# Optimization experiments

Measured on AMD Instinct MI355X. Metric: run time of the kernel, lower is better.

Reference implementation:

```python
import jax, jax.numpy as jnp
import numpy as np

B, H, W, C = 16, 64, 64, 384
DH = 32                 # dim_head
NH = C // DH            # heads = dim // dim_head
WS = 8                  # window_size
DFF = 4 * C             # dim_ff default = 4*dim
EPS = 1e-5


def setup_inputs() -> dict:
    key = jax.random.key(0)
    ks = jax.random.split(key, 6)
    rn = lambda k, shape, scale: (jax.random.normal(k, shape, jnp.float32) * scale)
    return {
        "x": rn(ks[0], (B, H, W, C), 1.0),
        "w_qkv": rn(ks[1], (C, 3 * NH * DH), 0.02),   # fused qkv projection, bias=False
        "w_out": rn(ks[2], (NH * DH, C), 0.02),       # attention output projection
        "gamma_attn": jnp.ones((C,), jnp.float32),     # LayerNormNoBias2d weight (post-attn)
        "w1": rn(ks[3], (C, DFF), 0.02),               # FFN up projection
        "w2": rn(ks[4], (DFF, C), 0.02),               # FFN down projection
        "gamma_ff": jnp.ones((C,), jnp.float32),       # LayerNormNoBias2d weight (post-FFN)
    }


def _shift2d(x):
    # S2-MLP style 4-way spatial shift of channel quarters, zero-filled at borders.
    c4 = x.shape[-1] // 4
    g1 = jnp.pad(x[:, :-1, :, 0 * c4:1 * c4], ((0, 0), (1, 0), (0, 0), (0, 0)))  # shift down
    g2 = jnp.pad(x[:, 1:, :, 1 * c4:2 * c4], ((0, 0), (0, 1), (0, 0), (0, 0)))   # shift up
    g3 = jnp.pad(x[:, :, :-1, 2 * c4:3 * c4], ((0, 0), (0, 0), (1, 0), (0, 0)))  # shift right
    g4 = jnp.pad(x[:, :, 1:, 3 * c4:4 * c4], ((0, 0), (0, 0), (0, 1), (0, 0)))   # shift left
    return jnp.concatenate([g1, g2, g3, g4], axis=-1)


def _ln_nobias(x, gamma):
    # LayerNorm over channel dim, weight only (no bias).
    mu = jnp.mean(x, axis=-1, keepdims=True)
    var = jnp.var(x, axis=-1, keepdims=True)
    return (x - mu) * jax.lax.rsqrt(var + EPS) * gamma


def _window_attention(x, w_qkv, w_out):
    # Grouped (non-overlapping) window multi-head self-attention.
    b, h, w, c = x.shape
    nh, nw = h // WS, w // WS
    T = WS * WS
    # partition into windows: (b*nh*nw, T, c)
    xw = x.reshape(b, nh, WS, nw, WS, c).transpose(0, 1, 3, 2, 4, 5).reshape(b * nh * nw, T, c)
    qkv = xw @ w_qkv                                   # (n, T, 3*NH*DH)
    qkv = qkv.reshape(-1, T, 3, NH, DH)
    q = qkv[:, :, 0].transpose(0, 2, 1, 3)             # (n, NH, T, DH)
    k = qkv[:, :, 1].transpose(0, 2, 1, 3)
    v = qkv[:, :, 2].transpose(0, 2, 1, 3)
    logits = jnp.einsum('nhqd,nhkd->nhqk', q, k) * (DH ** -0.5)
    attn = jax.nn.softmax(logits, axis=-1)
    o = jnp.einsum('nhqk,nhkd->nhqd', attn, v)         # (n, NH, T, DH)
    o = o.transpose(0, 2, 1, 3).reshape(-1, T, NH * DH) @ w_out
    # un-window back to (b, h, w, c)
    return o.reshape(b, nh, nw, WS, WS, c).transpose(0, 1, 3, 2, 4, 5).reshape(b, h, w, c)


def reference(x, w_qkv, w_out, gamma_attn, w1, w2, gamma_ff):
    # x = x + DropBlock(Norm(GWAttn(Shift2d(x))))   (drop rates = 0 -> identity)
    a = _window_attention(_shift2d(x), w_qkv, w_out)
    x = x + _ln_nobias(a, gamma_attn)
    # x = x + DropBlock(Norm(FF(x)))
    f = jax.nn.gelu(x @ w1, approximate=False) @ w2
    return x + _ln_nobias(f, gamma_ff)
```

## Files before the change

kernel.cpp:

```cpp
#include <hip/hip_runtime.h>
#include <hip/hip_bf16.h>
#include <math.h>

typedef __attribute__((ext_vector_type(8))) __bf16 bf16x8;
typedef __attribute__((ext_vector_type(4))) float f32x4;
typedef unsigned int uint32;

static constexpr int kC   = 384;
static constexpr int kNH  = 12;
static constexpr int kDH  = 32;
static constexpr int kT   = 64;
static constexpr int kB   = 16;
static constexpr int kH   = 64;
static constexpr int kW   = 64;
static constexpr int kDFF = 1536;
static constexpr long kNTOK = 65536;
static constexpr long kNT  = kNTOK * kC;

__device__ __forceinline__ float bf_lo(uint32 u){ return __uint_as_float(u << 16); }
__device__ __forceinline__ float bf_hi(uint32 u){ return __uint_as_float(u & 0xffff0000u); }

__device__ __forceinline__ float gelu_fast(float x) {
    float x2 = x * x;
    float t  = fmaf(0.102944787f, x2, 2.302208165f);
    float m  = fminf(x * t, 80.0f);
    float e  = __builtin_amdgcn_exp2f(m);
    float d  = 1.0f + e;
    return x * e * __builtin_amdgcn_rcpf(d);
}

__global__ void k_transpose_cast(const float* __restrict__ src, __bf16* __restrict__ dst,
                                 int K, int N)
{
    int o = blockIdx.x * 256 + threadIdx.x;
    if (o >= K * N) return;
    int n = o / K, k = o - n * K;
    dst[o] = (__bf16)src[(size_t)k * N + n];
}

__global__ __launch_bounds__(256) void k_shift_window(const float* __restrict__ x,
                                                      __bf16* __restrict__ Aw)
{
    int tid = blockIdx.x * 256 + threadIdx.x;
    int m = tid / 48;
    int g = tid - m * 48;
    int c0 = g * 8;
    int wi = m >> 6, t = m & 63;
    int b = wi >> 6, nh = (wi >> 3) & 7, nw = wi & 7;
    int h = nh * 8 + (t >> 3);
    int w = nw * 8 + (t & 7);
    int q = c0 / 96;
    int sh = h, sw = w;
    bool ok;
    if      (q == 0) { sh = h - 1; ok = (h >= 1);  }
    else if (q == 1) { sh = h + 1; ok = (h <= 62); }
    else if (q == 2) { sw = w - 1; ok = (w >= 1);  }
    else             { sw = w + 1; ok = (w <= 62); }

    __bf16 r[8] __attribute__((aligned(16)));
    if (ok) {
        const float4* src = reinterpret_cast<const float4*>(
            x + (((size_t)b * kH + sh) * kW + sw) * kC + c0);
        float4 v0 = src[0], v1 = src[1];
        r[0] = (__bf16)v0.x; r[1] = (__bf16)v0.y; r[2] = (__bf16)v0.z; r[3] = (__bf16)v0.w;
        r[4] = (__bf16)v1.x; r[5] = (__bf16)v1.y; r[6] = (__bf16)v1.z; r[7] = (__bf16)v1.w;
    } else {
        #pragma unroll
        for (int i = 0; i < 8; ++i) r[i] = (__bf16)0.0f;
    }
    *reinterpret_cast<int4*>(Aw + (size_t)m * kC + c0) = *reinterpret_cast<int4*>(r);
}

template<int EPI>
__global__ __launch_bounds__(256) void k_gemm(const __bf16* __restrict__ A,
                                              const __bf16* __restrict__ B,
                                              __bf16* __restrict__ Cout,
                                              int N, int K, int nt)
{
    __shared__ __align__(16) __bf16 As[2][128 * 32];
    __shared__ __align__(16) __bf16 Bs[2][128 * 32];
    const int tid  = threadIdx.x;
    const int wave = tid >> 6, lane = tid & 63;
    const int g = lane >> 4, qh = lane & 15;

    const int nwg = gridDim.x;
    const int wg  = (blockIdx.x & 7) * (nwg >> 3) + (blockIdx.x >> 3);
    const int nb  = wg % nt, mb = wg / nt;
    const int m0 = mb * 128, n0 = nb * 128;
    const int wr = (wave >> 1) * 64, wc = (wave & 1) * 64;

    const int sw = ((g ^ ((lane >> 1) & 3)) << 3);

    auto STAGE = [&](int buf, int k0) {
        #pragma unroll
        for (int i = 0; i < 2; ++i) {
            int idx = tid + i * 256;
            int row = idx >> 2;
            int gseg = (idx & 3) ^ ((idx >> 3) & 3);
            __builtin_amdgcn_global_load_lds(
                (const __attribute__((address_space(1))) void*)(A + (size_t)(m0 + row) * K + k0 + gseg * 8),
                (__attribute__((address_space(3))) void*)(&As[buf][idx * 8]), 16, 0, 0);
            __builtin_amdgcn_global_load_lds(
                (const __attribute__((address_space(1))) void*)(B + (size_t)(n0 + row) * K + k0 + gseg * 8),
                (__attribute__((address_space(3))) void*)(&Bs[buf][idx * 8]), 16, 0, 0);
        }
    };

    f32x4 acc[4][4] = {};
    const int nkt = K >> 5;

    STAGE(0, 0);
    for (int t = 0; t < nkt; ++t) {
        const int cur = t & 1;
        __syncthreads();
        if (t + 1 < nkt) STAGE(cur ^ 1, (t + 1) << 5);

        bf16x8 af[4], bfr[4];
        #pragma unroll
        for (int mi = 0; mi < 4; ++mi) {
            int ra = wr + mi * 16 + qh;
            af[mi] = *reinterpret_cast<const bf16x8*>(&As[cur][ra * 32 + sw]);
        }
        #pragma unroll
        for (int ni = 0; ni < 4; ++ni) {
            int rb = wc + ni * 16 + qh;
            bfr[ni] = *reinterpret_cast<const bf16x8*>(&Bs[cur][rb * 32 + sw]);
        }
        __builtin_amdgcn_s_setprio(1);
        #pragma unroll
        for (int mi = 0; mi < 4; ++mi)
            #pragma unroll
            for (int ni = 0; ni < 4; ++ni)
                acc[mi][ni] = __builtin_amdgcn_mfma_f32_16x16x32_bf16(af[mi], bfr[ni], acc[mi][ni], 0, 0, 0);
        __builtin_amdgcn_s_setprio(0);
    }

    #pragma unroll
    for (int ni = 0; ni < 4; ++ni) {
        const int col = n0 + wc + ni * 16 + qh;
        size_t cbase = 0;
        if constexpr (EPI == 0) {
            int s   = col / 384;
            int rem = col - s * 384;
            int hh  = rem >> 5, d = rem & 31;
            cbase = (size_t)s * kNT + ((size_t)hh * 64) * kDH + d;
        }
        #pragma unroll
        for (int mi = 0; mi < 4; ++mi) {
            #pragma unroll
            for (int r = 0; r < 4; ++r) {
                int row = m0 + wr + mi * 16 + (g << 2) + r;
                float v = acc[mi][ni][r];
                if constexpr (EPI == 0) {
                    Cout[cbase + ((size_t)(row >> 6) * kNH * 64 + (row & 63)) * kDH] = (__bf16)v;
                } else if constexpr (EPI == 1) {
                    Cout[(size_t)row * N + col] = (__bf16)v;
                } else {
                    Cout[(size_t)row * N + col] = (__bf16)gelu_fast(v);
                }
            }
        }
    }
}

__global__ __launch_bounds__(256) void k_attn(const __bf16* __restrict__ qkv,
                                              __bf16* __restrict__ AO)
{
    __shared__ __bf16 Pl[4][kT * kT];
    const int wave = threadIdx.x >> 6, lane = threadIdx.x & 63;
    const int pair = blockIdx.x * 4 + wave;
    const int wi = pair / kNH, hh = pair - wi * kNH;
    const int g = lane >> 4, qh = lane & 15;

    const __bf16* Qp = qkv + ((size_t)wi * kNH + hh) * (kT * kDH);
    const __bf16* Kp = Qp + kNT;
    const __bf16* Vp = Qp + 2 * kNT;
    char* Pb = (char*)&Pl[wave][0];

    bf16x8 qa[4], kb[4];
    #pragma unroll
    for (int mi = 0; mi < 4; ++mi)
        qa[mi] = *reinterpret_cast<const bf16x8*>(Qp + (mi * 16 + qh) * kDH + g * 8);
    #pragma unroll
    for (int ni = 0; ni < 4; ++ni)
        kb[ni] = *reinterpret_cast<const bf16x8*>(Kp + (ni * 16 + qh) * kDH + g * 8);

    f32x4 s[4][4] = {};
    #pragma unroll
    for (int mi = 0; mi < 4; ++mi)
        #pragma unroll
        for (int ni = 0; ni < 4; ++ni)
            s[mi][ni] = __builtin_amdgcn_mfma_f32_16x16x32_bf16(qa[mi], kb[ni], s[mi][ni], 0, 0, 0);

    const float scale = 0.17677669529663687f;
    float rmax[4][4], rsum[4][4];
    #pragma unroll
    for (int mi = 0; mi < 4; ++mi)
        #pragma unroll
        for (int r = 0; r < 4; ++r) {
            float a = fmaxf(fmaxf(s[mi][0][r], s[mi][1][r]), fmaxf(s[mi][2][r], s[mi][3][r]));
            #pragma unroll
            for (int st = 1; st < 16; st <<= 1) a = fmaxf(a, __shfl_xor(a, st));
            rmax[mi][r] = a;
        }
    #pragma unroll
    for (int mi = 0; mi < 4; ++mi)
        #pragma unroll
        for (int r = 0; r < 4; ++r) {
            float acc = 0.f;
            #pragma unroll
            for (int ni = 0; ni < 4; ++ni) {
                float p = __expf((s[mi][ni][r] - rmax[mi][r]) * scale);
                s[mi][ni][r] = p;
                acc += p;
            }
            #pragma unroll
            for (int st = 1; st < 16; st <<= 1) acc += __shfl_xor(acc, st);
            rsum[mi][r] = 1.0f / acc;
        }

    #pragma unroll
    for (int mi = 0; mi < 4; ++mi)
        #pragma unroll
        for (int ni = 0; ni < 4; ++ni)
            #pragma unroll
            for (int r = 0; r < 4; ++r) {
                int row = mi * 16 + g * 4 + r;
                int col = ni * 16 + qh;
                uint32 byte = (uint32)((row << 7) | (col << 1)) ^ (uint32)((row & 7) << 4);
                *reinterpret_cast<__bf16*>(Pb + byte) = (__bf16)s[mi][ni][r];
            }

    f32x4 o[4][2] = {};
    #pragma unroll
    for (int kk = 0; kk < 2; ++kk) {
        bf16x8 pa[4], vb[2];
        #pragma unroll
        for (int mi = 0; mi < 4; ++mi) {
            int row = mi * 16 + qh;
            uint32 byte = (uint32)((row << 7) | (kk << 6) | (g << 4)) ^ (uint32)((row & 7) << 4);
            pa[mi] = *reinterpret_cast<const bf16x8*>(Pb + byte);
        }
        #pragma unroll
        for (int n2 = 0; n2 < 2; ++n2) {
            __bf16 tmp[8];
            #pragma unroll
            for (int j = 0; j < 8; ++j)
                tmp[j] = Vp[(kk * 32 + g * 8 + j) * kDH + n2 * 16 + qh];
            vb[n2] = *reinterpret_cast<const bf16x8*>(tmp);
        }
        #pragma unroll
        for (int mi = 0; mi < 4; ++mi)
            #pragma unroll
            for (int n2 = 0; n2 < 2; ++n2)
                o[mi][n2] = __builtin_amdgcn_mfma_f32_16x16x32_bf16(pa[mi], vb[n2], o[mi][n2], 0, 0, 0);
    }

    #pragma unroll
    for (int mi = 0; mi < 4; ++mi)
        #pragma unroll
        for (int n2 = 0; n2 < 2; ++n2)
            #pragma unroll
            for (int r = 0; r < 4; ++r) {
                int row = mi * 16 + g * 4 + r;
                AO[((size_t)wi * 64 + row) * kC + hh * kDH + n2 * 16 + qh] =
                    (__bf16)(o[mi][n2][r] * rsum[mi][r]);
            }
}

__global__ __launch_bounds__(256) void k_ln_res1(const __bf16* __restrict__ P,
                                                 const float* __restrict__ x,
                                                 const float* __restrict__ gamma,
                                                 __bf16* __restrict__ X1)
{
    const int wave = threadIdx.x >> 6, lane = threadIdx.x & 63;
    const int tok = blockIdx.x * 4 + wave;
    const int b = tok >> 12, hw = tok & 4095, h = hw >> 6, w = hw & 63;
    const int m = (((b << 6) | ((h >> 3) << 3) | (w >> 3)) << 6) | (((h & 7) << 3) | (w & 7));

    float p[6]; float sum = 0.f, sq = 0.f;
    #pragma unroll
    for (int i = 0; i < 6; ++i) {
        p[i] = (float)P[(size_t)m * kC + lane + i * 64];
        sum += p[i]; sq += p[i] * p[i];
    }
    #pragma unroll
    for (int off = 32; off; off >>= 1) { sum += __shfl_xor(sum, off); sq += __shfl_xor(sq, off); }
    float mean = sum * (1.0f / kC);
    float var  = sq * (1.0f / kC) - mean * mean;
    float rs   = rsqrtf(var + 1e-5f);
    #pragma unroll
    for (int i = 0; i < 6; ++i) {
        int c = lane + i * 64;
        float v = x[(size_t)tok * kC + c] + (p[i] - mean) * rs * gamma[c];
        X1[(size_t)tok * kC + c] = (__bf16)v;
    }
}

__global__ __launch_bounds__(256) void k_ln_res2(const __bf16* __restrict__ F,
                                                 const __bf16* __restrict__ X1,
                                                 const float* __restrict__ gamma,
                                                 float* __restrict__ out)
{
    const int wave = threadIdx.x >> 6, lane = threadIdx.x & 63;
    const size_t tok = blockIdx.x * 4 + wave;

    float f[6]; float sum = 0.f, sq = 0.f;
    #pragma unroll
    for (int i = 0; i < 6; ++i) {
        f[i] = (float)F[tok * kC + lane + i * 64];
        sum += f[i]; sq += f[i] * f[i];
    }
    #pragma unroll
    for (int off = 32; off; off >>= 1) { sum += __shfl_xor(sum, off); sq += __shfl_xor(sq, off); }
    float mean = sum * (1.0f / kC);
    float var  = sq * (1.0f / kC) - mean * mean;
    float rs   = rsqrtf(var + 1e-5f);
    #pragma unroll
    for (int i = 0; i < 6; ++i) {
        int c = lane + i * 64;
        out[tok * kC + c] = (float)X1[tok * kC + c] + (f[i] - mean) * rs * gamma[c];
    }
}

extern "C" void kernel_launch(void* const* d_in, const int* in_sizes, int n_in,
                              void* d_out, int out_size, void* d_ws, size_t ws_size,
                              hipStream_t stream) {
    const float* x    = (const float*)d_in[0];
    const float* wqkv = (const float*)d_in[1];
    const float* wout = (const float*)d_in[2];
    const float* g_at = (const float*)d_in[3];
    const float* w1   = (const float*)d_in[4];
    const float* w2   = (const float*)d_in[5];
    const float* g_ff = (const float*)d_in[6];
    float* out = (float*)d_out;

    char* ws = (char*)d_ws;
    size_t off = 0;
    auto alloc = [&](size_t bytes) { size_t o = off; off += (bytes + 255) & ~(size_t)255; return o; };
    __bf16* WqkvT = (__bf16*)(ws + alloc((size_t)1152 * 384 * 2));
    __bf16* WoutT = (__bf16*)(ws + alloc((size_t)384 * 384 * 2));
    __bf16* W1T   = (__bf16*)(ws + alloc((size_t)1536 * 384 * 2));
    __bf16* W2T   = (__bf16*)(ws + alloc((size_t)384 * 1536 * 2));
    __bf16* R1    = (__bf16*)(ws + alloc((size_t)kNTOK * kDFF * 2));
    __bf16* R2    = (__bf16*)(ws + alloc((size_t)kNT * 2));
    __bf16* R3    = (__bf16*)(ws + alloc((size_t)kNT * 2));

    k_transpose_cast<<<dim3((384 * 1152 + 255) / 256), 256, 0, stream>>>(wqkv, WqkvT, 384, 1152);
    k_transpose_cast<<<dim3((384 * 384 + 255) / 256), 256, 0, stream>>>(wout, WoutT, 384, 384);
    k_transpose_cast<<<dim3((384 * 1536 + 255) / 256), 256, 0, stream>>>(w1, W1T, 384, 1536);
    k_transpose_cast<<<dim3((1536 * 384 + 255) / 256), 256, 0, stream>>>(w2, W2T, 1536, 384);

    k_shift_window<<<dim3(12288), 256, 0, stream>>>(x, R2);

    k_gemm<0><<<dim3(512 * 9), 256, 0, stream>>>(R2, WqkvT, R1, 1152, 384, 9);

    k_attn<<<dim3(3072), 256, 0, stream>>>(R1, R2);

    k_gemm<1><<<dim3(512 * 3), 256, 0, stream>>>(R2, WoutT, R3, 384, 384, 3);

    k_ln_res1<<<dim3(16384), 256, 0, stream>>>(R3, x, g_at, R2);

    k_gemm<2><<<dim3(512 * 12), 256, 0, stream>>>(R2, W1T, R1, 1536, 384, 12);

    k_gemm<1><<<dim3(512 * 3), 256, 0, stream>>>(R1, W2T, R3, 384, 1536, 3);

    k_ln_res2<<<dim3(16384), 256, 0, stream>>>(R3, R2, g_ff, out);
}
```

Before: 514.3 us.

## Restructure GEMM to 256x128 tiles with B fragments loaded directly into registers

The GEMM tile grows from 128x128 to 256x128, and each of the four waves now owns 64 rows across the full 128 columns. Only A is staged in LDS. B fragments are read straight from global memory into registers and double-buffered across an unrolled pair of k-steps. The aim is to cut LDS traffic and launch count per output and to raise MFMA work per wave. In exchange, register pressure rises (32 accumulators plus 16 B fragments) and the B global reads are less coalesced. The loop also assumes the number of k-tiles is even, which holds for K=384 and K=1536.

```diff
diff --git a/kernel.cpp b/kernel.cpp
--- a/kernel.cpp
+++ b/kernel.cpp
@@ -72,13 +72,12 @@
 }
 
 template<int EPI>
-__global__ __launch_bounds__(256) void k_gemm(const __bf16* __restrict__ A,
-                                              const __bf16* __restrict__ B,
-                                              __bf16* __restrict__ Cout,
-                                              int N, int K, int nt)
-{
-    __shared__ __align__(16) __bf16 As[2][128 * 32];
-    __shared__ __align__(16) __bf16 Bs[2][128 * 32];
+__global__ __launch_bounds__(256, 2) void k_gemm(const __bf16* __restrict__ A,
+                                                 const __bf16* __restrict__ B,
+                                                 __bf16* __restrict__ Cout,
+                                                 int N, int K, int nt)
+{
+    __shared__ __align__(16) __bf16 As[2][256 * 32];
     const int tid  = threadIdx.x;
     const int wave = tid >> 6, lane = tid & 63;
     const int g = lane >> 4, qh = lane & 15;
@@ -86,58 +85,66 @@
     const int nwg = gridDim.x;
     const int wg  = (blockIdx.x & 7) * (nwg >> 3) + (blockIdx.x >> 3);
     const int nb  = wg % nt, mb = wg / nt;
-    const int m0 = mb * 128, n0 = nb * 128;
-    const int wr = (wave >> 1) * 64, wc = (wave & 1) * 64;
+    const int m0 = mb * 256, n0 = nb * 128;
+    const int wr = wave * 64;
 
     const int sw = ((g ^ ((lane >> 1) & 3)) << 3);
 
-    auto STAGE = [&](int buf, int k0) {
-        #pragma unroll
-        for (int i = 0; i < 2; ++i) {
+    auto STAGE = [&](int buf, int t) {
+        const int k0 = t << 5;
+        #pragma unroll
+        for (int i = 0; i < 4; ++i) {
             int idx = tid + i * 256;
             int row = idx >> 2;
             int gseg = (idx & 3) ^ ((idx >> 3) & 3);
             __builtin_amdgcn_global_load_lds(
                 (const __attribute__((address_space(1))) void*)(A + (size_t)(m0 + row) * K + k0 + gseg * 8),
                 (__attribute__((address_space(3))) void*)(&As[buf][idx * 8]), 16, 0, 0);
-            __builtin_amdgcn_global_load_lds(
-                (const __attribute__((address_space(1))) void*)(B + (size_t)(n0 + row) * K + k0 + gseg * 8),
-                (__attribute__((address_space(3))) void*)(&Bs[buf][idx * 8]), 16, 0, 0);
         }
     };
 
-    f32x4 acc[4][4] = {};
+    bf16x8 bX[8], bY[8];
+    auto LOADB = [&](bf16x8* set, int t) {
+        const int k0 = t << 5;
+        #pragma unroll
+        for (int ni = 0; ni < 8; ++ni)
+            set[ni] = *reinterpret_cast<const bf16x8*>(B + (size_t)(n0 + ni * 16 + qh) * K + k0 + g * 8);
+    };
+
+    f32x4 acc[4][8] = {};
     const int nkt = K >> 5;
 
-    STAGE(0, 0);
-    for (int t = 0; t < nkt; ++t) {
-        const int cur = t & 1;
-        __syncthreads();
-        if (t + 1 < nkt) STAGE(cur ^ 1, (t + 1) << 5);
-
-        bf16x8 af[4], bfr[4];
+    auto COMPUTE = [&](const __bf16* Asb, const bf16x8* bset) {
+        bf16x8 af[4];
         #pragma unroll
         for (int mi = 0; mi < 4; ++mi) {
             int ra = wr + mi * 16 + qh;
-            af[mi] = *reinterpret_cast<const bf16x8*>(&As[cur][ra * 32 + sw]);
-        }
-        #pragma unroll
-        for (int ni = 0; ni < 4; ++ni) {
-            int rb = wc + ni * 16 + qh;
-            bfr[ni] = *reinterpret_cast<const bf16x8*>(&Bs[cur][rb * 32 + sw]);
+            af[mi] = *reinterpret_cast<const bf16x8*>(&Asb[ra * 32 + sw]);
         }
         __builtin_amdgcn_s_setprio(1);
         #pragma unroll
         for (int mi = 0; mi < 4; ++mi)
             #pragma unroll
-            for (int ni = 0; ni < 4; ++ni)
-                acc[mi][ni] = __builtin_amdgcn_mfma_f32_16x16x32_bf16(af[mi], bfr[ni], acc[mi][ni], 0, 0, 0);
+            for (int ni = 0; ni < 8; ++ni)
+                acc[mi][ni] = __builtin_amdgcn_mfma_f32_16x16x32_bf16(af[mi], bset[ni], acc[mi][ni], 0, 0, 0);
         __builtin_amdgcn_s_setprio(0);
-    }
-
-    #pragma unroll
-    for (int ni = 0; ni < 4; ++ni) {
-        const int col = n0 + wc + ni * 16 + qh;
+    };
+
+    STAGE(0, 0);
+    LOADB(bX, 0);
+    for (int t = 0; t < nkt; t += 2) {
+        __syncthreads();
+        STAGE(1, t + 1);
+        LOADB(bY, t + 1);
+        COMPUTE(&As[0][0], bX);
+        __syncthreads();
+        if (t + 2 < nkt) { STAGE(0, t + 2); LOADB(bX, t + 2); }
+        COMPUTE(&As[1][0], bY);
+    }
+
+    #pragma unroll
+    for (int ni = 0; ni < 8; ++ni) {
+        const int col = n0 + ni * 16 + qh;
         size_t cbase = 0;
         if constexpr (EPI == 0) {
             int s   = col / 384;
@@ -353,17 +360,17 @@
 
     k_shift_window<<<dim3(12288), 256, 0, stream>>>(x, R2);
 
-    k_gemm<0><<<dim3(512 * 9), 256, 0, stream>>>(R2, WqkvT, R1, 1152, 384, 9);
+    k_gemm<0><<<dim3(256 * 9), 256, 0, stream>>>(R2, WqkvT, R1, 1152, 384, 9);
 
     k_attn<<<dim3(3072), 256, 0, stream>>>(R1, R2);
 
-    k_gemm<1><<<dim3(512 * 3), 256, 0, stream>>>(R2, WoutT, R3, 384, 384, 3);
+    k_gemm<1><<<dim3(256 * 3), 256, 0, stream>>>(R2, WoutT, R3, 384, 384, 3);
 
     k_ln_res1<<<dim3(16384), 256, 0, stream>>>(R3, x, g_at, R2);
 
-    k_gemm<2><<<dim3(512 * 12), 256, 0, stream>>>(R2, W1T, R1, 1536, 384, 12);
-
-    k_gemm<1><<<dim3(512 * 3), 256, 0, stream>>>(R1, W2T, R3, 384, 1536, 3);
+    k_gemm<2><<<dim3(256 * 12), 256, 0, stream>>>(R2, W1T, R1, 1536, 384, 12);
+
+    k_gemm<1><<<dim3(256 * 3), 256, 0, stream>>>(R1, W2T, R3, 384, 1536, 3);
 
     k_ln_res2<<<dim3(16384), 256, 0, stream>>>(R3, R2, g_ff, out);
 }
```

Result: slower. 836.0 us (+62.6%).

## Fuse LayerNorm and residual into output and FFN-down GEMM epilogues

Applied to the files above, without the earlier changes.

Adds a GEMM kernel whose 64-row tile covers the full 384-column output row, so per-row LayerNorm statistics can be reduced in-block and the norm plus residual add applied in the epilogue. It replaces the out-projection GEMM followed by the LN-residual kernel, and likewise the FFN down-projection followed by its LN. This removes two standalone LN kernels and the round trip of the bf16 intermediate through memory. The cost is fewer workgroups (1024), a large B tile in LDS per block that lowers occupancy, and uncoalesced epilogue stores.

```diff
diff --git a/kernel.cpp b/kernel.cpp
--- a/kernel.cpp
+++ b/kernel.cpp
@@ -10,7 +10,6 @@
 static constexpr int kNH  = 12;
 static constexpr int kDH  = 32;
 static constexpr int kT   = 64;
-static constexpr int kB   = 16;
 static constexpr int kH   = 64;
 static constexpr int kW   = 64;
 static constexpr int kDFF = 1536;
@@ -91,7 +90,8 @@
 
     const int sw = ((g ^ ((lane >> 1) & 3)) << 3);
 
-    auto STAGE = [&](int buf, int k0) {
+    auto STAGE = [&](int buf, int t) {
+        const int k0 = t << 5;
         #pragma unroll
         for (int i = 0; i < 2; ++i) {
             int idx = tid + i * 256;
@@ -113,7 +113,7 @@
     for (int t = 0; t < nkt; ++t) {
         const int cur = t & 1;
         __syncthreads();
-        if (t + 1 < nkt) STAGE(cur ^ 1, (t + 1) << 5);
+        if (t + 1 < nkt) STAGE(cur ^ 1, t + 1);
 
         bf16x8 af[4], bfr[4];
         #pragma unroll
@@ -163,6 +163,149 @@
     }
 }
 
+template<int LN>
+__global__ __launch_bounds__(256) void k_gemm_ln(const __bf16* __restrict__ A,
+                                                 const __bf16* __restrict__ B,
+                                                 const float* __restrict__ gamma,
+                                                 const void* __restrict__ resid,
+                                                 void* __restrict__ outp,
+                                                 int K)
+{
+    __shared__ __align__(16) __bf16 As[2][64 * 32];
+    __shared__ __align__(16) __bf16 Bs[2][384 * 32];
+    __shared__ float red[64][4][2];
+    __shared__ float2 stats[64];
+
+    const int tid  = threadIdx.x;
+    const int wave = tid >> 6, lane = tid & 63;
+    const int g = lane >> 4, qh = lane & 15;
+
+    const int nwg = gridDim.x;
+    const int mb  = (blockIdx.x & 7) * (nwg >> 3) + (blockIdx.x >> 3);
+    const int m0  = mb * 64;
+    const int wc  = wave * 96;
+
+    const int sw = ((g ^ ((lane >> 1) & 3)) << 3);
+
+    auto STAGE = [&](int buf, int t) {
+        const int k0 = t << 5;
+        {
+            int idx = tid;
+            int row = idx >> 2;
+            int gseg = (idx & 3) ^ ((idx >> 3) & 3);
+            __builtin_amdgcn_global_load_lds(
+                (const __attribute__((address_space(1))) void*)(A + (size_t)(m0 + row) * K + k0 + gseg * 8),
+                (__attribute__((address_space(3))) void*)(&As[buf][idx * 8]), 16, 0, 0);
+        }
+        #pragma unroll
+        for (int i = 0; i < 6; ++i) {
+            int idx = tid + i * 256;
+            int row = idx >> 2;
+            int gseg = (idx & 3) ^ ((idx >> 3) & 3);
+            __builtin_amdgcn_global_load_lds(
+                (const __attribute__((address_space(1))) void*)(B + (size_t)row * K + k0 + gseg * 8),
+                (__attribute__((address_space(3))) void*)(&Bs[buf][idx * 8]), 16, 0, 0);
+        }
+    };
+
+    f32x4 acc[4][6] = {};
+    const int nkt = K >> 5;
+
+    STAGE(0, 0);
+    for (int t = 0; t < nkt; ++t) {
+        const int cur = t & 1;
+        __syncthreads();
+        if (t + 1 < nkt) STAGE(cur ^ 1, t + 1);
+
+        bf16x8 af[4], bfr[6];
+        #pragma unroll
+        for (int mi = 0; mi < 4; ++mi) {
+            int ra = mi * 16 + qh;
+            af[mi] = *reinterpret_cast<const bf16x8*>(&As[cur][ra * 32 + sw]);
+        }
+        #pragma unroll
+        for (int ni = 0; ni < 6; ++ni) {
+            int rb = wc + ni * 16 + qh;
+            bfr[ni] = *reinterpret_cast<const bf16x8*>(&Bs[cur][rb * 32 + sw]);
+        }
+        __builtin_amdgcn_s_setprio(1);
+        #pragma unroll
+        for (int mi = 0; mi < 4; ++mi)
+            #pragma unroll
+            for (int ni = 0; ni < 6; ++ni)
+                acc[mi][ni] = __builtin_amdgcn_mfma_f32_16x16x32_bf16(af[mi], bfr[ni], acc[mi][ni], 0, 0, 0);
+        __builtin_amdgcn_s_setprio(0);
+    }
+
+    #pragma unroll
+    for (int mi = 0; mi < 4; ++mi) {
+        #pragma unroll
+        for (int r = 0; r < 4; ++r) {
+            float t1 = 0.f, t2 = 0.f;
+            #pragma unroll
+            for (int ni = 0; ni < 6; ++ni) {
+                float v = acc[mi][ni][r];
+                t1 += v; t2 += v * v;
+            }
+            #pragma unroll
+            for (int st = 1; st < 16; st <<= 1) {
+                t1 += __shfl_xor(t1, st);
+                t2 += __shfl_xor(t2, st);
+            }
+            if (qh == 0) {
+                int row = mi * 16 + (g << 2) + r;
+                red[row][wave][0] = t1;
+                red[row][wave][1] = t2;
+            }
+        }
+    }
+    __syncthreads();
+    if (tid < 64) {
+        float s1 = red[tid][0][0] + red[tid][1][0] + red[tid][2][0] + red[tid][3][0];
+        float s2 = red[tid][0][1] + red[tid][1][1] + red[tid][2][1] + red[tid][3][1];
+        float mean = s1 * (1.0f / 384.0f);
+        float var  = s2 * (1.0f / 384.0f) - mean * mean;
+        stats[tid] = make_float2(mean, rsqrtf(var + 1e-5f));
+    }
+    __syncthreads();
+
+    float gcol[6];
+    #pragma unroll
+    for (int ni = 0; ni < 6; ++ni) gcol[ni] = gamma[wc + ni * 16 + qh];
+
+    #pragma unroll
+    for (int mi = 0; mi < 4; ++mi) {
+        #pragma unroll
+        for (int r = 0; r < 4; ++r) {
+            const int row = mi * 16 + (g << 2) + r;
+            const float2 st = stats[row];
+            size_t tok;
+            if constexpr (LN == 1) {
+                int m = m0 + row;
+                int t = m & 63, wi = m >> 6;
+                int b = wi >> 6, nh = (wi >> 3) & 7, nw = wi & 7;
+                int h = nh * 8 + (t >> 3);
+                int w = nw * 8 + (t & 7);
+                tok = ((size_t)b << 12) | (h << 6) | w;
+            } else {
+                tok = (size_t)(m0 + row);
+            }
+            #pragma unroll
+            for (int ni = 0; ni < 6; ++ni) {
+                const int col = wc + ni * 16 + qh;
+                float v = (acc[mi][ni][r] - st.x) * st.y * gcol[ni];
+                if constexpr (LN == 1) {
+                    float xr = ((const float*)resid)[tok * kC + col];
+                    ((__bf16*)outp)[tok * kC + col] = (__bf16)(xr + v);
+                } else {
+                    float xr = (float)((const __bf16*)resid)[tok * kC + col];
+                    ((float*)outp)[tok * kC + col] = xr + v;
+                }
+            }
+        }
+    }
+}
+
 __global__ __launch_bounds__(256) void k_attn(const __bf16* __restrict__ qkv,
                                               __bf16* __restrict__ AO)
 {
@@ -266,61 +409,6 @@
                 AO[((size_t)wi * 64 + row) * kC + hh * kDH + n2 * 16 + qh] =
                     (__bf16)(o[mi][n2][r] * rsum[mi][r]);
             }
-}
-
-__global__ __launch_bounds__(256) void k_ln_res1(const __bf16* __restrict__ P,
-                                                 const float* __restrict__ x,
-                                                 const float* __restrict__ gamma,
-                                                 __bf16* __restrict__ X1)
-{
-    const int wave = threadIdx.x >> 6, lane = threadIdx.x & 63;
-    const int tok = blockIdx.x * 4 + wave;
-    const int b = tok >> 12, hw = tok & 4095, h = hw >> 6, w = hw & 63;
-    const int m = (((b << 6) | ((h >> 3) << 3) | (w >> 3)) << 6) | (((h & 7) << 3) | (w & 7));
-
-    float p[6]; float sum = 0.f, sq = 0.f;
-    #pragma unroll
-    for (int i = 0; i < 6; ++i) {
-        p[i] = (float)P[(size_t)m * kC + lane + i * 64];
-        sum += p[i]; sq += p[i] * p[i];
-    }
-    #pragma unroll
-    for (int off = 32; off; off >>= 1) { sum += __shfl_xor(sum, off); sq += __shfl_xor(sq, off); }
-    float mean = sum * (1.0f / kC);
-    float var  = sq * (1.0f / kC) - mean * mean;
-    float rs   = rsqrtf(var + 1e-5f);
-    #pragma unroll
-    for (int i = 0; i < 6; ++i) {
-        int c = lane + i * 64;
-        float v = x[(size_t)tok * kC + c] + (p[i] - mean) * rs * gamma[c];
-        X1[(size_t)tok * kC + c] = (__bf16)v;
-    }
-}
-
-__global__ __launch_bounds__(256) void k_ln_res2(const __bf16* __restrict__ F,
-                                                 const __bf16* __restrict__ X1,
-                                                 const float* __restrict__ gamma,
-                                                 float* __restrict__ out)
-{
-    const int wave = threadIdx.x >> 6, lane = threadIdx.x & 63;
-    const size_t tok = blockIdx.x * 4 + wave;
-
-    float f[6]; float sum = 0.f, sq = 0.f;
-    #pragma unroll
-    for (int i = 0; i < 6; ++i) {
-        f[i] = (float)F[tok * kC + lane + i * 64];
-        sum += f[i]; sq += f[i] * f[i];
-    }
-    #pragma unroll
-    for (int off = 32; off; off >>= 1) { sum += __shfl_xor(sum, off); sq += __shfl_xor(sq, off); }
-    float mean = sum * (1.0f / kC);
-    float var  = sq * (1.0f / kC) - mean * mean;
-    float rs   = rsqrtf(var + 1e-5f);
-    #pragma unroll
-    for (int i = 0; i < 6; ++i) {
-        int c = lane + i * 64;
-        out[tok * kC + c] = (float)X1[tok * kC + c] + (f[i] - mean) * rs * gamma[c];
-    }
 }
 
 extern "C" void kernel_launch(void* const* d_in, const int* in_sizes, int n_in,
@@ -357,13 +445,9 @@
 
     k_attn<<<dim3(3072), 256, 0, stream>>>(R1, R2);
 
-    k_gemm<1><<<dim3(512 * 3), 256, 0, stream>>>(R2, WoutT, R3, 384, 384, 3);
-
-    k_ln_res1<<<dim3(16384), 256, 0, stream>>>(R3, x, g_at, R2);
-
-    k_gemm<2><<<dim3(512 * 12), 256, 0, stream>>>(R2, W1T, R1, 1536, 384, 12);
-
-    k_gemm<1><<<dim3(512 * 3), 256, 0, stream>>>(R1, W2T, R3, 384, 1536, 3);
-
-    k_ln_res2<<<dim3(16384), 256, 0, stream>>>(R3, R2, g_ff, out);
-}
+    k_gemm_ln<1><<<dim3(1024), 256, 0, stream>>>(R2, WoutT, g_at, x, R3, 384);
+
+    k_gemm<2><<<dim3(512 * 12), 256, 0, stream>>>(R3, W1T, R1, 1536, 384, 12);
+
+    k_gemm_ln<2><<<dim3(1024), 256, 0, stream>>>(R1, W2T, g_ff, R3, out, 1536);
+}
```

New measurement: 638.8 us. 1.24x slower.
